# Kernel tuning notes

Measured on AMD Instinct MI355X. Metric: run time of the kernel, lower is better.

## Reference

```python
import jax, jax.numpy as jnp
import numpy as np

B = 256        # trees per batch
M = 1023       # nodes per tree (complete binary tree, depth 0..9)
N = B * M      # total flattened nodes
H = 128        # hidden dim
VOCAB = 100    # AST node-type vocab
NUM_CLASSES = 6
MAX_DEPTH = 10 # levels 0..9


def setup_inputs() -> dict:
    key = jax.random.key(0)
    k1, k2, k3, k4 = jax.random.split(key, 4)
    i = np.arange(M)
    parent_local = np.maximum((i - 1) // 2, 0)          # root points to itself
    depth_local = np.floor(np.log2(i + 1)).astype(np.int64)
    tree_off = np.arange(B, dtype=np.int64) * M
    parent_idx = (parent_local[None, :] + tree_off[:, None]).reshape(-1)
    depth = np.tile(depth_local, B)
    root_idx = tree_off
    return {
        "node_type": jax.random.randint(k1, (N,), 0, VOCAB, dtype=jnp.int64),
        "parent_idx": jnp.asarray(parent_idx),
        "depth": jnp.asarray(depth),
        "root_idx": jnp.asarray(root_idx),
        "E": jax.random.normal(k2, (VOCAB, H), dtype=jnp.float32) * 0.1,
        "Wh": jax.random.normal(k3, (H, H), dtype=jnp.float32) * (1.0 / np.sqrt(H)),
        "bh": jnp.zeros((H,), dtype=jnp.float32),
        "Wc": jax.random.normal(k4, (H, NUM_CLASSES), dtype=jnp.float32) * (1.0 / np.sqrt(H)),
        "bc": jnp.zeros((NUM_CLASSES,), dtype=jnp.float32),
    }


def reference(node_type, parent_idx, depth, root_idx, E, Wh, bh, Wc, bc):
    # Feature extraction: ast_class -> vector (Ast2VectorForPython analog)
    x = E[node_type]                         # [N, H]
    h = jnp.tanh(x)                          # leaves start from their own embedding
    # Leaf-to-root recursive propagation, one level at a time (children first).
    for d in range(MAX_DEPTH - 1, 0, -1):
        child_h = jnp.where((depth == d)[:, None], h, 0.0)
        agg = jax.ops.segment_sum(child_h, parent_idx, num_segments=N)  # [N, H]
        upd = jnp.tanh(x + agg @ Wh + bh)
        h = jnp.where((depth == d - 1)[:, None], upd, h)
    h_root = h[root_idx]                     # [B, H] == torch.stack(outputs, 0)
    logits = h_root @ Wc + bc                # nn.Linear(128, 6)
    return jax.nn.log_softmax(logits, axis=-1)
```

## Files before the change

### kernel.cpp

```cpp
#include <hip/hip_runtime.h>

#define TREES    256
#define MNODES   1023
#define HD       128
#define VOCAB_SZ 100
#define NCLS     6
#define NTHR     1024

typedef __attribute__((ext_vector_type(8))) short  short8;
typedef __attribute__((ext_vector_type(4))) unsigned short ushort4_t;
typedef __attribute__((ext_vector_type(4))) __bf16 bf16x4;
typedef __attribute__((ext_vector_type(8))) __bf16 bf16x8;
typedef __attribute__((ext_vector_type(4))) float  f32x4;

__device__ __forceinline__ unsigned short bfc(float f) {
    return __builtin_bit_cast(unsigned short, (__bf16)f);
}
__device__ __forceinline__ float bf2f(unsigned short s) {
    return __uint_as_float(((unsigned int)s) << 16);
}
__device__ __forceinline__ float fast_tanh(float x) {
    float e = __expf(2.0f * x);
    return 1.0f - 2.0f / (e + 1.0f);
}

#define OFF_R1    0
#define OFF_R2    32768
#define OFF_ETBL  65536
#define OFF_NT    91136
#define OFF_HROOT 92160
#define LDS_BYTES 92672

template<int P, int MODE>
__device__ __forceinline__ void level_phase(
    unsigned char* lds, const unsigned char* bin, unsigned char* bout,
    const bf16x8 (&aT)[8], const unsigned char* nt, int Loff,
    int cw, int l16, int lg, int g, float* hroot)
{
    constexpr int NBT = (P + 15) / 16;
    for (int bt = g; bt < NBT; bt += 4) {
        const int pb = bt * 16;
        const int p  = pb + l16;
        const int pc = (p < P) ? p : (P - 1);
        const int bswz = (pc & 7) << 4;
        bf16x8 bfrag[4];
#pragma unroll
        for (int kt = 0; kt < 4; ++kt)
            bfrag[kt] = __builtin_bit_cast(bf16x8,
                *(const short8*)(bin + pc * 256 + ((kt * 64 + lg * 16) ^ bswz)));
        f32x4 acc0 = {0.f, 0.f, 0.f, 0.f};
        f32x4 acc1 = {0.f, 0.f, 0.f, 0.f};
#pragma unroll
        for (int kt = 0; kt < 4; ++kt) {
            acc0 = __builtin_amdgcn_mfma_f32_16x16x32_bf16(aT[kt],     bfrag[kt], acc0, 0, 0, 0);
            acc1 = __builtin_amdgcn_mfma_f32_16x16x32_bf16(aT[4 + kt], bfrag[kt], acc1, 0, 0, 0);
        }
        const int ty   = nt[Loff + pc];
        const int tswz = (ty & 7) << 4;
        float h[8];
#pragma unroll
        for (int n2 = 0; n2 < 2; ++n2) {
            const int n0 = cw * 32 + n2 * 16 + lg * 4;
            const uint2 ev = *(const uint2*)(lds + OFF_ETBL + ty * 256 + ((n0 * 2) ^ tswz));
            const f32x4 a = n2 ? acc1 : acc0;
            h[n2*4+0] = fast_tanh(bf2f((unsigned short)(ev.x & 0xffffu)) + a[0]);
            h[n2*4+1] = fast_tanh(bf2f((unsigned short)(ev.x >> 16))     + a[1]);
            h[n2*4+2] = fast_tanh(bf2f((unsigned short)(ev.y & 0xffffu)) + a[2]);
            h[n2*4+3] = fast_tanh(bf2f((unsigned short)(ev.y >> 16))     + a[3]);
        }
        if (MODE == 1) {
            if (l16 == 0) {
#pragma unroll
                for (int n2 = 0; n2 < 2; ++n2) {
                    const int n0 = cw * 32 + n2 * 16 + lg * 4;
                    float4 v = {h[n2*4+0], h[n2*4+1], h[n2*4+2], h[n2*4+3]};
                    *(float4*)(hroot + n0) = v;
                }
            }
        } else {
#pragma unroll
            for (int u = 0; u < 8; ++u) h[u] += __shfl_xor(h[u], 1, 64);
            if ((p < P) && !(l16 & 1)) {
                const int orow = (pb >> 1) + (l16 >> 1);
                const int oswz = (orow & 7) << 4;
#pragma unroll
                for (int n2 = 0; n2 < 2; ++n2) {
                    const int n0 = cw * 32 + n2 * 16 + lg * 4;
                    bf16x4 pk = {(__bf16)h[n2*4+0], (__bf16)h[n2*4+1],
                                 (__bf16)h[n2*4+2], (__bf16)h[n2*4+3]};
                    *(bf16x4*)(bout + orow * 256 + ((n0 * 2) ^ oswz)) = pk;
                }
            }
        }
    }
}

__global__ __launch_bounds__(NTHR, 4)
void tree_rnn_kernel(const int* __restrict__ node_type,
                     const float* __restrict__ E,
                     const float* __restrict__ Wh,
                     const float* __restrict__ bh,
                     const float* __restrict__ Wc,
                     const float* __restrict__ bc,
                     float* __restrict__ out)
{
    __shared__ __align__(16) unsigned char lds[LDS_BYTES];
    unsigned char* nt    = (unsigned char*)(lds + OFF_NT);
    float*         hroot = (float*)(lds + OFF_HROOT);

    const int t    = blockIdx.x;
    const int tid  = threadIdx.x;
    const int lane = tid & 63;
    const int wv   = tid >> 6;
    const int l16  = lane & 15;
    const int lg   = lane >> 4;
    const int cw   = wv & 3;
    const int g    = wv >> 2;

    if (tid < MNODES) nt[tid] = (unsigned char)node_type[t * MNODES + tid];
    for (int i4 = tid; i4 < VOCAB_SZ * HD / 4; i4 += NTHR) {
        int row = i4 >> 5, c4 = i4 & 31;
        float4 v  = ((const float4*)E)[i4];
        float4 bv = ((const float4*)bh)[c4];
        ushort4_t e, te;
        e[0] = bfc(v.x + bv.x); e[1] = bfc(v.y + bv.y);
        e[2] = bfc(v.z + bv.z); e[3] = bfc(v.w + bv.w);
        te[0] = bfc(fast_tanh(v.x)); te[1] = bfc(fast_tanh(v.y));
        te[2] = bfc(fast_tanh(v.z)); te[3] = bfc(fast_tanh(v.w));
        int boff = row * 256 + ((c4 * 8) ^ ((row & 7) << 4));
        *(ushort4_t*)(lds + OFF_ETBL + boff) = e;
        *(ushort4_t*)(lds + OFF_R1   + boff) = te;
    }
    for (int i4 = tid; i4 < HD * HD / 4; i4 += NTHR) {
        int k  = i4 >> 5;
        int n0 = (i4 & 31) * 4;
        float4 v = ((const float4*)Wh)[i4];
        float vv[4] = {v.x, v.y, v.z, v.w};
#pragma unroll
        for (int j = 0; j < 4; ++j) {
            int n = n0 + j;
            *(unsigned short*)(lds + OFF_R2 + n * 256 + ((k * 2) ^ ((n & 7) << 4))) = bfc(vv[j]);
        }
    }
    __syncthreads();

    bf16x8 aT[8];
#pragma unroll
    for (int n2 = 0; n2 < 2; ++n2) {
        const int ncol = cw * 32 + n2 * 16 + l16;
        const int nswz = (ncol & 7) << 4;
#pragma unroll
        for (int kt = 0; kt < 4; ++kt)
            aT[n2 * 4 + kt] = __builtin_bit_cast(bf16x8,
                *(const short8*)(lds + OFF_R2 + ncol * 256 + ((kt * 64 + lg * 16) ^ nswz)));
    }
    __syncthreads();

    for (int bt = g; bt < 7; bt += 4) {
        const int tyr = bt * 16 + l16;
        const int tyc = (tyr < VOCAB_SZ) ? tyr : (VOCAB_SZ - 1);
        const int bswz = (tyc & 7) << 4;
        bf16x8 bfrag[4];
#pragma unroll
        for (int kt = 0; kt < 4; ++kt)
            bfrag[kt] = __builtin_bit_cast(bf16x8,
                *(const short8*)(lds + OFF_R1 + tyc * 256 + ((kt * 64 + lg * 16) ^ bswz)));
        f32x4 acc0 = {0.f, 0.f, 0.f, 0.f};
        f32x4 acc1 = {0.f, 0.f, 0.f, 0.f};
#pragma unroll
        for (int kt = 0; kt < 4; ++kt) {
            acc0 = __builtin_amdgcn_mfma_f32_16x16x32_bf16(aT[kt],     bfrag[kt], acc0, 0, 0, 0);
            acc1 = __builtin_amdgcn_mfma_f32_16x16x32_bf16(aT[4 + kt], bfrag[kt], acc1, 0, 0, 0);
        }
        if (tyr < VOCAB_SZ) {
            const int tswz = (tyr & 7) << 4;
#pragma unroll
            for (int n2 = 0; n2 < 2; ++n2) {
                const f32x4 a = n2 ? acc1 : acc0;
                const int n0 = cw * 32 + n2 * 16 + lg * 4;
                bf16x4 pk = {(__bf16)a[0], (__bf16)a[1], (__bf16)a[2], (__bf16)a[3]};
                *(bf16x4*)(lds + OFF_R2 + tyr * 256 + ((n0 * 2) ^ tswz)) = pk;
            }
        }
    }
    __syncthreads();

#pragma unroll
    for (int it = 0; it < 2; ++it) {
        const int idx = it * NTHR + tid;
        const int j   = idx >> 4;
        const int c8  = idx & 15;
        const int colb = c8 * 16;
        const int o8  = 255 + 2 * j;
        const int o9  = 511 + 4 * j;
        int tyP0 = nt[o8], tyP1 = nt[o8 + 1];
        int tyAL = nt[o9], tyAR = nt[o9 + 1], tyBL = nt[o9 + 2], tyBR = nt[o9 + 3];
        short8 e0  = *(const short8*)(lds + OFF_ETBL + tyP0 * 256 + (colb ^ ((tyP0 & 7) << 4)));
        short8 e1  = *(const short8*)(lds + OFF_ETBL + tyP1 * 256 + (colb ^ ((tyP1 & 7) << 4)));
        short8 gAL = *(const short8*)(lds + OFF_R2   + tyAL * 256 + (colb ^ ((tyAL & 7) << 4)));
        short8 gAR = *(const short8*)(lds + OFF_R2   + tyAR * 256 + (colb ^ ((tyAR & 7) << 4)));
        short8 gBL = *(const short8*)(lds + OFF_R2   + tyBL * 256 + (colb ^ ((tyBL & 7) << 4)));
        short8 gBR = *(const short8*)(lds + OFF_R2   + tyBR * 256 + (colb ^ ((tyBR & 7) << 4)));
        short8 o;
#pragma unroll
        for (int u = 0; u < 8; ++u) {
            float hA = fast_tanh(bf2f((unsigned short)e0[u]) + bf2f((unsigned short)gAL[u]) +
                                 bf2f((unsigned short)gAR[u]));
            float hB = fast_tanh(bf2f((unsigned short)e1[u]) + bf2f((unsigned short)gBL[u]) +
                                 bf2f((unsigned short)gBR[u]));
            o[u] = (short)bfc(hA + hB);
        }
        *(short8*)(lds + OFF_R1 + j * 256 + (colb ^ ((j & 7) << 4))) = o;
    }
    __syncthreads();

    unsigned char* R1 = lds + OFF_R1;
    unsigned char* R2 = lds + OFF_R2;
    level_phase<128, 0>(lds, R1, R2, aT, nt, 127, cw, l16, lg, g, hroot); __syncthreads();
    level_phase< 64, 0>(lds, R2, R1, aT, nt,  63, cw, l16, lg, g, hroot); __syncthreads();
    level_phase< 32, 0>(lds, R1, R2, aT, nt,  31, cw, l16, lg, g, hroot); __syncthreads();
    level_phase< 16, 0>(lds, R2, R1, aT, nt,  15, cw, l16, lg, g, hroot); __syncthreads();
    level_phase<  8, 0>(lds, R1, R2, aT, nt,   7, cw, l16, lg, g, hroot); __syncthreads();
    level_phase<  4, 0>(lds, R2, R1, aT, nt,   3, cw, l16, lg, g, hroot); __syncthreads();
    level_phase<  2, 0>(lds, R1, R2, aT, nt,   1, cw, l16, lg, g, hroot); __syncthreads();
    level_phase<  1, 1>(lds, R2, R1, aT, nt,   0, cw, l16, lg, g, hroot); __syncthreads();

    if (tid < 64) {
        float hA = hroot[tid];
        float hB = hroot[tid + 64];
        float lgt[NCLS];
#pragma unroll
        for (int c = 0; c < NCLS; ++c) {
            float v = hA * Wc[tid * NCLS + c] + hB * Wc[(tid + 64) * NCLS + c];
#pragma unroll
            for (int off = 32; off > 0; off >>= 1)
                v += __shfl_xor(v, off, 64);
            lgt[c] = v + bc[c];
        }
        if (tid == 0) {
            float mx = lgt[0];
#pragma unroll
            for (int c = 1; c < NCLS; ++c) mx = fmaxf(mx, lgt[c]);
            float s = 0.f;
#pragma unroll
            for (int c = 0; c < NCLS; ++c) s += __expf(lgt[c] - mx);
            float lse = mx + __logf(s);
#pragma unroll
            for (int c = 0; c < NCLS; ++c) out[t * NCLS + c] = lgt[c] - lse;
        }
    }
}

extern "C" void kernel_launch(void* const* d_in, const int* in_sizes, int n_in,
                              void* d_out, int out_size, void* d_ws, size_t ws_size,
                              hipStream_t stream) {
    const int*   node_type = (const int*)d_in[0];
    const float* E  = (const float*)d_in[4];
    const float* Wh = (const float*)d_in[5];
    const float* bh = (const float*)d_in[6];
    const float* Wc = (const float*)d_in[7];
    const float* bc = (const float*)d_in[8];
    float* out = (float*)d_out;
    tree_rnn_kernel<<<dim3(TREES), dim3(NTHR), 0, stream>>>(node_type, E, Wh, bh, Wc, bc, out);
}
```

Before: 26.76 us.

## Run small tree levels on a single wavefront to drop block barriers

After the two widest levels, all waves except wave 0 exit. Wave 0 then processes levels 32 down to 1 by itself, reading the full transposed Wh from a new dedicated LDS region, so no __syncthreads is needed between those levels. The aim is to remove six block-wide barriers on phases that have very little work. In exchange, LDS use grows from about 92 KB to about 118 KB, which can lower occupancy, and the tail is serialized onto one wave that reloads Wh fragments from LDS.

```diff
diff --git a/kernel.cpp b/kernel.cpp
--- a/kernel.cpp
+++ b/kernel.cpp
@@ -25,17 +25,18 @@
 }
 
 #define OFF_R1    0
-#define OFF_R2    32768
-#define OFF_ETBL  65536
-#define OFF_NT    91136
-#define OFF_HROOT 92160
-#define LDS_BYTES 92672
-
-template<int P, int MODE>
+#define OFF_GW    32768
+#define OFF_WHT   58368
+#define OFF_ETBL  91136
+#define OFF_NT    116736
+#define OFF_HROOT 117760
+#define LDS_BYTES 118272
+
+template<int P>
 __device__ __forceinline__ void level_phase(
     unsigned char* lds, const unsigned char* bin, unsigned char* bout,
     const bf16x8 (&aT)[8], const unsigned char* nt, int Loff,
-    int cw, int l16, int lg, int g, float* hroot)
+    int cw, int l16, int lg, int g)
 {
     constexpr int NBT = (P + 15) / 16;
     for (int bt = g; bt < NBT; bt += 4) {
@@ -68,26 +69,71 @@
             h[n2*4+2] = fast_tanh(bf2f((unsigned short)(ev.y & 0xffffu)) + a[2]);
             h[n2*4+3] = fast_tanh(bf2f((unsigned short)(ev.y >> 16))     + a[3]);
         }
-        if (MODE == 1) {
-            if (l16 == 0) {
-#pragma unroll
-                for (int n2 = 0; n2 < 2; ++n2) {
-                    const int n0 = cw * 32 + n2 * 16 + lg * 4;
-                    float4 v = {h[n2*4+0], h[n2*4+1], h[n2*4+2], h[n2*4+3]};
+#pragma unroll
+        for (int u = 0; u < 8; ++u) h[u] += __shfl_xor(h[u], 1, 64);
+        if ((p < P) && !(l16 & 1)) {
+            const int orow = (pb >> 1) + (l16 >> 1);
+            const int oswz = (orow & 7) << 4;
+#pragma unroll
+            for (int n2 = 0; n2 < 2; ++n2) {
+                const int n0 = cw * 32 + n2 * 16 + lg * 4;
+                bf16x4 pk = {(__bf16)h[n2*4+0], (__bf16)h[n2*4+1],
+                             (__bf16)h[n2*4+2], (__bf16)h[n2*4+3]};
+                *(bf16x4*)(bout + orow * 256 + ((n0 * 2) ^ oswz)) = pk;
+            }
+        }
+    }
+}
+
+template<int P>
+__device__ __forceinline__ void tail_level(
+    unsigned char* lds, const unsigned char* bin, unsigned char* bout,
+    const unsigned char* nt, int Loff, int l16, int lg, float* hroot)
+{
+    constexpr int NBT = (P + 15) / 16;
+#pragma unroll
+    for (int bt = 0; bt < NBT; ++bt) {
+        const int p  = bt * 16 + l16;
+        const int pc = (p < P) ? p : (P - 1);
+        const int bswz = (pc & 7) << 4;
+        bf16x8 bfrag[4];
+#pragma unroll
+        for (int kt = 0; kt < 4; ++kt)
+            bfrag[kt] = __builtin_bit_cast(bf16x8,
+                *(const short8*)(bin + pc * 256 + ((kt * 64 + lg * 16) ^ bswz)));
+        const int ty   = nt[Loff + pc];
+        const int tswz = (ty & 7) << 4;
+        const int orow = (bt << 3) + (l16 >> 1);
+        const int oswz = (orow & 7) << 4;
+#pragma unroll
+        for (int n8 = 0; n8 < 8; ++n8) {
+            const int ncol = n8 * 16 + l16;
+            const int nswz = (ncol & 7) << 4;
+            f32x4 acc = {0.f, 0.f, 0.f, 0.f};
+#pragma unroll
+            for (int kt = 0; kt < 4; ++kt) {
+                bf16x8 a = __builtin_bit_cast(bf16x8,
+                    *(const short8*)(lds + OFF_WHT + ncol * 256 + ((kt * 64 + lg * 16) ^ nswz)));
+                acc = __builtin_amdgcn_mfma_f32_16x16x32_bf16(a, bfrag[kt], acc, 0, 0, 0);
+            }
+            const int n0 = n8 * 16 + lg * 4;
+            const uint2 ev = *(const uint2*)(lds + OFF_ETBL + ty * 256 + ((n0 * 2) ^ tswz));
+            float h0 = fast_tanh(bf2f((unsigned short)(ev.x & 0xffffu)) + acc[0]);
+            float h1 = fast_tanh(bf2f((unsigned short)(ev.x >> 16))     + acc[1]);
+            float h2 = fast_tanh(bf2f((unsigned short)(ev.y & 0xffffu)) + acc[2]);
+            float h3 = fast_tanh(bf2f((unsigned short)(ev.y >> 16))     + acc[3]);
+            if (P == 1) {
+                if (l16 == 0) {
+                    float4 v = {h0, h1, h2, h3};
                     *(float4*)(hroot + n0) = v;
                 }
-            }
-        } else {
-#pragma unroll
-            for (int u = 0; u < 8; ++u) h[u] += __shfl_xor(h[u], 1, 64);
-            if ((p < P) && !(l16 & 1)) {
-                const int orow = (pb >> 1) + (l16 >> 1);
-                const int oswz = (orow & 7) << 4;
-#pragma unroll
-                for (int n2 = 0; n2 < 2; ++n2) {
-                    const int n0 = cw * 32 + n2 * 16 + lg * 4;
-                    bf16x4 pk = {(__bf16)h[n2*4+0], (__bf16)h[n2*4+1],
-                                 (__bf16)h[n2*4+2], (__bf16)h[n2*4+3]};
+            } else {
+                h0 += __shfl_xor(h0, 1, 64);
+                h1 += __shfl_xor(h1, 1, 64);
+                h2 += __shfl_xor(h2, 1, 64);
+                h3 += __shfl_xor(h3, 1, 64);
+                if ((p < P) && !(l16 & 1)) {
+                    bf16x4 pk = {(__bf16)h0, (__bf16)h1, (__bf16)h2, (__bf16)h3};
                     *(bf16x4*)(bout + orow * 256 + ((n0 * 2) ^ oswz)) = pk;
                 }
             }
@@ -139,7 +185,7 @@
 #pragma unroll
         for (int j = 0; j < 4; ++j) {
             int n = n0 + j;
-            *(unsigned short*)(lds + OFF_R2 + n * 256 + ((k * 2) ^ ((n & 7) << 4))) = bfc(vv[j]);
+            *(unsigned short*)(lds + OFF_WHT + n * 256 + ((k * 2) ^ ((n & 7) << 4))) = bfc(vv[j]);
         }
     }
     __syncthreads();
@@ -152,10 +198,8 @@
 #pragma unroll
         for (int kt = 0; kt < 4; ++kt)
             aT[n2 * 4 + kt] = __builtin_bit_cast(bf16x8,
-                *(const short8*)(lds + OFF_R2 + ncol * 256 + ((kt * 64 + lg * 16) ^ nswz)));
-    }
-    __syncthreads();
-
+                *(const short8*)(lds + OFF_WHT + ncol * 256 + ((kt * 64 + lg * 16) ^ nswz)));
+    }
     for (int bt = g; bt < 7; bt += 4) {
         const int tyr = bt * 16 + l16;
         const int tyc = (tyr < VOCAB_SZ) ? tyr : (VOCAB_SZ - 1);
@@ -179,7 +223,7 @@
                 const f32x4 a = n2 ? acc1 : acc0;
                 const int n0 = cw * 32 + n2 * 16 + lg * 4;
                 bf16x4 pk = {(__bf16)a[0], (__bf16)a[1], (__bf16)a[2], (__bf16)a[3]};
-                *(bf16x4*)(lds + OFF_R2 + tyr * 256 + ((n0 * 2) ^ tswz)) = pk;
+                *(bf16x4*)(lds + OFF_GW + tyr * 256 + ((n0 * 2) ^ tswz)) = pk;
             }
         }
     }
@@ -197,10 +241,10 @@
         int tyAL = nt[o9], tyAR = nt[o9 + 1], tyBL = nt[o9 + 2], tyBR = nt[o9 + 3];
         short8 e0  = *(const short8*)(lds + OFF_ETBL + tyP0 * 256 + (colb ^ ((tyP0 & 7) << 4)));
         short8 e1  = *(const short8*)(lds + OFF_ETBL + tyP1 * 256 + (colb ^ ((tyP1 & 7) << 4)));
-        short8 gAL = *(const short8*)(lds + OFF_R2   + tyAL * 256 + (colb ^ ((tyAL & 7) << 4)));
-        short8 gAR = *(const short8*)(lds + OFF_R2   + tyAR * 256 + (colb ^ ((tyAR & 7) << 4)));
-        short8 gBL = *(const short8*)(lds + OFF_R2   + tyBL * 256 + (colb ^ ((tyBL & 7) << 4)));
-        short8 gBR = *(const short8*)(lds + OFF_R2   + tyBR * 256 + (colb ^ ((tyBR & 7) << 4)));
+        short8 gAL = *(const short8*)(lds + OFF_GW   + tyAL * 256 + (colb ^ ((tyAL & 7) << 4)));
+        short8 gAR = *(const short8*)(lds + OFF_GW   + tyAR * 256 + (colb ^ ((tyAR & 7) << 4)));
+        short8 gBL = *(const short8*)(lds + OFF_GW   + tyBL * 256 + (colb ^ ((tyBL & 7) << 4)));
+        short8 gBR = *(const short8*)(lds + OFF_GW   + tyBR * 256 + (colb ^ ((tyBR & 7) << 4)));
         short8 o;
 #pragma unroll
         for (int u = 0; u < 8; ++u) {
@@ -214,30 +258,33 @@
     }
     __syncthreads();
 
-    unsigned char* R1 = lds + OFF_R1;
-    unsigned char* R2 = lds + OFF_R2;
-    level_phase<128, 0>(lds, R1, R2, aT, nt, 127, cw, l16, lg, g, hroot); __syncthreads();
-    level_phase< 64, 0>(lds, R2, R1, aT, nt,  63, cw, l16, lg, g, hroot); __syncthreads();
-    level_phase< 32, 0>(lds, R1, R2, aT, nt,  31, cw, l16, lg, g, hroot); __syncthreads();
-    level_phase< 16, 0>(lds, R2, R1, aT, nt,  15, cw, l16, lg, g, hroot); __syncthreads();
-    level_phase<  8, 0>(lds, R1, R2, aT, nt,   7, cw, l16, lg, g, hroot); __syncthreads();
-    level_phase<  4, 0>(lds, R2, R1, aT, nt,   3, cw, l16, lg, g, hroot); __syncthreads();
-    level_phase<  2, 0>(lds, R1, R2, aT, nt,   1, cw, l16, lg, g, hroot); __syncthreads();
-    level_phase<  1, 1>(lds, R2, R1, aT, nt,   0, cw, l16, lg, g, hroot); __syncthreads();
-
-    if (tid < 64) {
-        float hA = hroot[tid];
-        float hB = hroot[tid + 64];
+    unsigned char* R1   = lds + OFF_R1;
+    unsigned char* PONG = lds + OFF_GW;
+    level_phase<128>(lds, R1, PONG, aT, nt, 127, cw, l16, lg, g); __syncthreads();
+    level_phase< 64>(lds, PONG, R1, aT, nt,  63, cw, l16, lg, g); __syncthreads();
+
+    if (wv != 0) return;
+
+    tail_level<32>(lds, R1,   PONG, nt, 31, l16, lg, hroot);
+    tail_level<16>(lds, PONG, R1,   nt, 15, l16, lg, hroot);
+    tail_level< 8>(lds, R1,   PONG, nt,  7, l16, lg, hroot);
+    tail_level< 4>(lds, PONG, R1,   nt,  3, l16, lg, hroot);
+    tail_level< 2>(lds, R1,   PONG, nt,  1, l16, lg, hroot);
+    tail_level< 1>(lds, PONG, R1,   nt,  0, l16, lg, hroot);
+
+    {
+        float hA = hroot[lane];
+        float hB = hroot[lane + 64];
         float lgt[NCLS];
 #pragma unroll
         for (int c = 0; c < NCLS; ++c) {
-            float v = hA * Wc[tid * NCLS + c] + hB * Wc[(tid + 64) * NCLS + c];
+            float v = hA * Wc[lane * NCLS + c] + hB * Wc[(lane + 64) * NCLS + c];
 #pragma unroll
             for (int off = 32; off > 0; off >>= 1)
                 v += __shfl_xor(v, off, 64);
             lgt[c] = v + bc[c];
         }
-        if (tid == 0) {
+        if (lane == 0) {
             float mx = lgt[0];
 #pragma unroll
             for (int c = 1; c < NCLS; ++c) mx = fmaxf(mx, lgt[c]);
```

New measurement: 43.69 us. +63.2%, slower.
